# Kernel tuning notes

Hardware: AMD Instinct MI355X
Metric: run time of the kernel (lower is better)

Reference implementation:

```python
import jax, jax.numpy as jnp
import numpy as np

B, T, F = 2048, 256, 64
EMB, UNITS = 16, 32
CAT = UNITS + EMB  # concat([h, x]) -> 48


def setup_inputs() -> dict:
    key = jax.random.key(0)
    ks = jax.random.split(key, 12)
    s = lambda k, shape, fan: jax.random.normal(k, shape, jnp.float32) / np.sqrt(fan)
    return {
        "x": jax.random.normal(ks[0], (B, T, F), jnp.float32),
        "W_emb": s(ks[1], (F, EMB), F), "b_emb": jnp.zeros((EMB,), jnp.float32),
        "W_f": s(ks[2], (CAT, UNITS), CAT), "b_f": jnp.zeros((UNITS,), jnp.float32),
        "W_i": s(ks[3], (CAT, UNITS), CAT), "b_i": jnp.zeros((UNITS,), jnp.float32),
        "W_c": s(ks[4], (CAT, UNITS), CAT), "b_c": jnp.zeros((UNITS,), jnp.float32),
        "W_o": s(ks[5], (CAT, UNITS), CAT), "b_o": jnp.zeros((UNITS,), jnp.float32),
        "W_out": s(ks[6], (UNITS, 1), UNITS), "b_out": jnp.zeros((1,), jnp.float32),
    }


def reference(x, W_emb, b_emb, W_f, b_f, W_i, b_i, W_c, b_c, W_o, b_o, W_out, b_out):
    # embedding: Dense(16, sigmoid)
    e = jax.nn.sigmoid(jnp.einsum('btf,fe->bte', x, W_emb) + b_emb)  # [B,T,EMB]
    e_t = jnp.swapaxes(e, 0, 1)  # [T,B,EMB] for scan

    h0 = jnp.zeros((x.shape[0], UNITS), jnp.float32)
    c0 = jnp.zeros((x.shape[0], UNITS), jnp.float32)

    # fuse 4 gate Dense layers into one GEMM per step (same math)
    W_gates = jnp.concatenate([W_f, W_i, W_c, W_o], axis=1)  # [CAT, 4*UNITS]
    b_gates = jnp.concatenate([b_f, b_i, b_c, b_o], axis=0)

    def step(carry, x_t):
        h, c = carry
        z = jnp.concatenate([h, x_t], axis=-1)  # concat([h_t, x_t])
        g = z @ W_gates + b_gates  # [B, 4*UNITS]
        f = jax.nn.sigmoid(g[:, :UNITS])
        i = jax.nn.sigmoid(g[:, UNITS:2 * UNITS])
        ch = jnp.tanh(g[:, 2 * UNITS:3 * UNITS])
        o = jax.nn.sigmoid(g[:, 3 * UNITS:])
        c_new = f * c + i * ch
        h_new = o * jnp.tanh(c_new)
        return (h_new, c_new), None

    (h_last, _), _ = jax.lax.scan(step, (h0, c0), e_t)
    return jax.nn.sigmoid(h_last @ W_out + b_out)  # [B,1]
```

## Files before the change

### kernel.cpp

```cpp
#include <hip/hip_runtime.h>

#define B_ 2048
#define T_ 256
#define F_ 64
#define EMB_ 16
#define UNITS_ 32
#define L2E 1.44269504f

typedef __attribute__((ext_vector_type(8))) short bf16x8;
typedef __attribute__((ext_vector_type(4))) float f32x4;

__device__ __forceinline__ unsigned short f2bf(float f) {
    unsigned u = __float_as_uint(f);
    return (unsigned short)((u + 0x7FFFu + ((u >> 16) & 1u)) >> 16);
}
__device__ __forceinline__ float fast_sigmoid(float x) {
    return __builtin_amdgcn_rcpf(1.0f + __builtin_amdgcn_exp2f(-L2E * x));
}

__global__ __launch_bounds__(64) void embed_mfma(
    const float* __restrict__ x, const float* __restrict__ Wemb,
    const float* __restrict__ bemb, unsigned int* __restrict__ e_ws)
{
    __shared__ unsigned short slab[2][16][72];

    const int lane = threadIdx.x;
    const int g = lane >> 4, c = lane & 15;
    const int tile = blockIdx.x >> 5;
    const int t0 = (blockIdx.x & 31) * 8;

    bf16x8 A1, A2;
    #pragma unroll
    for (int j = 0; j < 4; ++j) {
        A1[j]     = (short)f2bf(Wemb[(4 * g + j) * EMB_ + c]);
        A1[j + 4] = (short)f2bf(Wemb[(16 + 4 * g + j) * EMB_ + c]);
        A2[j]     = (short)f2bf(Wemb[(32 + 4 * g + j) * EMB_ + c]);
        A2[j + 4] = (short)f2bf(Wemb[(48 + 4 * g + j) * EMB_ + c]);
    }
    f32x4 bc;
    #pragma unroll
    for (int r = 0; r < 4; ++r) bc[r] = bemb[4 * g + r];

    const int sr = lane >> 2, sc = lane & 3;
    const float* xs = x + (size_t)(tile * 16 + sr) * T_ * F_ + sc * 16;

    float4 rld[4], nld[4];
    {
        const float4* p = (const float4*)(xs + (size_t)t0 * F_);
        rld[0] = p[0]; rld[1] = p[1]; rld[2] = p[2]; rld[3] = p[3];
    }

    #pragma unroll
    for (int i = 0; i < 9; ++i) {
        if (i < 7) {
            const float4* p = (const float4*)(xs + (size_t)(t0 + i + 1) * F_);
            nld[0] = p[0]; nld[1] = p[1]; nld[2] = p[2]; nld[3] = p[3];
        }
        if (i < 8) {
            const float* f = (const float*)rld;
            unsigned u[8];
            #pragma unroll
            for (int k = 0; k < 8; ++k)
                u[k] = (unsigned)f2bf(f[2 * k]) | ((unsigned)f2bf(f[2 * k + 1]) << 16);
            uint4* d = (uint4*)&slab[i & 1][sr][sc * 16];
            d[0] = make_uint4(u[0], u[1], u[2], u[3]);
            d[1] = make_uint4(u[4], u[5], u[6], u[7]);
        }
        if (i > 0) {
            const unsigned short* row = &slab[(i - 1) & 1][c][0];
            ushort4 l1 = *(const ushort4*)(row + 4 * g);
            ushort4 h1 = *(const ushort4*)(row + 16 + 4 * g);
            ushort4 l2 = *(const ushort4*)(row + 32 + 4 * g);
            ushort4 h2 = *(const ushort4*)(row + 48 + 4 * g);
            bf16x8 B1 = {(short)l1.x, (short)l1.y, (short)l1.z, (short)l1.w,
                         (short)h1.x, (short)h1.y, (short)h1.z, (short)h1.w};
            bf16x8 B2 = {(short)l2.x, (short)l2.y, (short)l2.z, (short)l2.w,
                         (short)h2.x, (short)h2.y, (short)h2.z, (short)h2.w};
            f32x4 acc = __builtin_amdgcn_mfma_f32_16x16x32_bf16(A1, B1, bc, 0, 0, 0);
            acc = __builtin_amdgcn_mfma_f32_16x16x32_bf16(A2, B2, acc, 0, 0, 0);
            unsigned u0 = (unsigned)f2bf(fast_sigmoid(acc[0])) |
                          ((unsigned)f2bf(fast_sigmoid(acc[1])) << 16);
            unsigned u1 = (unsigned)f2bf(fast_sigmoid(acc[2])) |
                          ((unsigned)f2bf(fast_sigmoid(acc[3])) << 16);
            size_t idx = (((size_t)tile * T_ + (t0 + i - 1)) * 64 + lane) * 2;
            *(uint2*)(e_ws + idx) = make_uint2(u0, u1);
        }
        #pragma unroll
        for (int k = 0; k < 4; ++k) rld[k] = nld[k];
    }
}

__global__ __launch_bounds__(256) void lstm_rec(
    const float* __restrict__ Wf, const float* __restrict__ bfv,
    const float* __restrict__ Wi, const float* __restrict__ biv,
    const float* __restrict__ Wc, const float* __restrict__ bcv,
    const float* __restrict__ Wo, const float* __restrict__ bov,
    const float* __restrict__ Wout, const float* __restrict__ bout,
    const unsigned int* __restrict__ e_ws, float* __restrict__ out)
{
    __shared__ unsigned short hx[2][16][36];
    __shared__ float pred[4][16];

    const int tid = threadIdx.x;
    const int w = tid >> 6;
    const int lane = tid & 63;
    const int g = lane >> 4, m15 = lane & 15;
    const int bt = blockIdx.x;

    const int gate = m15 & 3;
    const float* Wsel = (gate == 0) ? Wf : (gate == 1) ? Wi : (gate == 2) ? Wc : Wo;
    const float ascale = (gate == 2) ? (-2.0f * L2E) : (-L2E);
    const int uAb = 8 * w + 2 * (m15 >> 2);

    bf16x8 Ah[2], Ae[2];
    #pragma unroll
    for (int tau = 0; tau < 2; ++tau) {
        const int uA = uAb + tau;
        #pragma unroll
        for (int j = 0; j < 4; ++j) {
            Ah[tau][j]     = (short)f2bf(ascale * Wsel[(4 * g + j) * UNITS_ + uA]);
            Ah[tau][j + 4] = (short)f2bf(ascale * Wsel[(16 + 4 * g + j) * UNITS_ + uA]);
            Ae[tau][j]     = (short)f2bf(ascale * Wsel[(32 + 4 * g + j) * UNITS_ + uA]);
            Ae[tau][j + 4] = 0;
        }
    }
    f32x4 bias[2];
    #pragma unroll
    for (int tau = 0; tau < 2; ++tau) {
        const int u = 8 * w + 2 * g + tau;
        bias[tau][0] = -L2E * bfv[u];
        bias[tau][1] = -L2E * biv[u];
        bias[tau][2] = -2.0f * L2E * bcv[u];
        bias[tau][3] = -L2E * bov[u];
    }

    const uint2* ep = (const uint2*)e_ws + (size_t)bt * T_ * 64 + lane;
    uint2 ering[4];
    #pragma unroll
    for (int s = 0; s < 4; ++s) ering[s] = ep[(size_t)s * 64];

    for (int i = tid; i < 2 * 16 * 36 / 2; i += 256) ((unsigned*)hx)[i] = 0;
    __syncthreads();

    float c0 = 0.f, c1 = 0.f, hf0 = 0.f, hf1 = 0.f;

    auto cell = [&](const f32x4& acc, float& cst, float& hf) {
        float Ef = __builtin_amdgcn_exp2f(acc[0]);
        float Ei = __builtin_amdgcn_exp2f(acc[1]);
        float Ec = __builtin_amdgcn_exp2f(acc[2]);
        float Eo = __builtin_amdgcn_exp2f(acc[3]);
        float Pf = 1.f + Ef, Pi = 1.f + Ei, Pc = 1.f + Ec, Po = 1.f + Eo;
        float Mc = 1.f - Ec;
        float t1 = Pi * Pc;
        float num = fmaf(cst, t1, Pf * Mc);
        float den = Pf * t1;
        float cn = num * __builtin_amdgcn_rcpf(den);
        cst = cn;
        float Eh = __builtin_amdgcn_exp2f(cn * (-2.0f * L2E));
        float Mh = 1.f - Eh;
        float d2 = (1.f + Eh) * Po;
        hf = Mh * __builtin_amdgcn_rcpf(d2);
    };

    f32x4 Fe0, Fe1;
    {
        uint2 ev = ering[0];
        bf16x8 Be = {(short)(ev.x & 0xffff), (short)(ev.x >> 16),
                     (short)(ev.y & 0xffff), (short)(ev.y >> 16), 0, 0, 0, 0};
        Fe0 = __builtin_amdgcn_mfma_f32_16x16x32_bf16(Ae[0], Be, bias[0], 0, 0, 0);
        Fe1 = __builtin_amdgcn_mfma_f32_16x16x32_bf16(Ae[1], Be, bias[1], 0, 0, 0);
    }

    #pragma unroll 1
    for (int t = 0; t < T_; t += 4) {
        #pragma unroll
        for (int s = 0; s < 4; ++s) {
            const int u = t + s;
            const unsigned short* hrow = &hx[u & 1][m15][0];
            ushort4 hlo = *(const ushort4*)(hrow + 4 * g);
            ushort4 hhi = *(const ushort4*)(hrow + 16 + 4 * g);
            bf16x8 Bh = {(short)hlo.x, (short)hlo.y, (short)hlo.z, (short)hlo.w,
                         (short)hhi.x, (short)hhi.y, (short)hhi.z, (short)hhi.w};
            f32x4 a0 = __builtin_amdgcn_mfma_f32_16x16x32_bf16(Ah[0], Bh, Fe0, 0, 0, 0);
            f32x4 a1 = __builtin_amdgcn_mfma_f32_16x16x32_bf16(Ah[1], Bh, Fe1, 0, 0, 0);

            int tn = (u + 4 < T_) ? u + 4 : T_ - 1;
            uint2 ev = ering[(s + 1) & 3];
            ering[s] = ep[(size_t)tn * 64];
            bf16x8 Be = {(short)(ev.x & 0xffff), (short)(ev.x >> 16),
                         (short)(ev.y & 0xffff), (short)(ev.y >> 16), 0, 0, 0, 0};
            Fe0 = __builtin_amdgcn_mfma_f32_16x16x32_bf16(Ae[0], Be, bias[0], 0, 0, 0);
            Fe1 = __builtin_amdgcn_mfma_f32_16x16x32_bf16(Ae[1], Be, bias[1], 0, 0, 0);

            cell(a0, c0, hf0);
            cell(a1, c1, hf1);
            unsigned pk;
            asm("v_cvt_pk_bf16_f32 %0, %1, %2" : "=v"(pk) : "v"(hf0), "v"(hf1));
            *(unsigned*)&hx[(u + 1) & 1][m15][8 * w + 2 * g] = pk;

            asm volatile("s_waitcnt lgkmcnt(0)\n\ts_barrier" ::: "memory");
        }
    }

    float p = hf0 * Wout[8 * w + 2 * g] + hf1 * Wout[8 * w + 2 * g + 1];
    p += __shfl_xor(p, 16, 64);
    p += __shfl_xor(p, 32, 64);
    if (lane < 16) pred[w][lane] = p;
    __syncthreads();
    if (tid < 16)
        out[bt * 16 + tid] = fast_sigmoid(pred[0][tid] + pred[1][tid] +
                                          pred[2][tid] + pred[3][tid] + bout[0]);
}

extern "C" void kernel_launch(void* const* d_in, const int* in_sizes, int n_in,
                              void* d_out, int out_size, void* d_ws, size_t ws_size,
                              hipStream_t stream) {
    const float* x    = (const float*)d_in[0];
    const float* Wemb = (const float*)d_in[1];
    const float* bemb = (const float*)d_in[2];
    const float* Wf   = (const float*)d_in[3];
    const float* bfv  = (const float*)d_in[4];
    const float* Wi   = (const float*)d_in[5];
    const float* biv  = (const float*)d_in[6];
    const float* Wc   = (const float*)d_in[7];
    const float* bcv  = (const float*)d_in[8];
    const float* Wo   = (const float*)d_in[9];
    const float* bov  = (const float*)d_in[10];
    const float* Wout = (const float*)d_in[11];
    const float* bout = (const float*)d_in[12];
    float* out = (float*)d_out;
    unsigned int* e_ws = (unsigned int*)d_ws;

    hipLaunchKernelGGL(embed_mfma, dim3(128 * 32), dim3(64), 0, stream,
                       x, Wemb, bemb, e_ws);
    hipLaunchKernelGGL(lstm_rec, dim3(B_ / 16), dim3(256), 0, stream,
                       Wf, bfv, Wi, biv, Wc, bcv, Wo, bov, Wout, bout,
                       (const unsigned int*)e_ws, out);
}
```

Baseline: 88.37 us.

## Interleave two independent batch tiles per LSTM block to increase ILP

Each recurrent block now processes two 16-row batch tiles with separate hidden/cell states, interleaving their MFMAs and cell math within each timestep and sharing one barrier per step. The grid is halved accordingly. The intent is to hide the serial MFMA/transcendental/barrier latency of the recurrence with independent work, at the cost of more registers per thread and fewer active blocks across the GPU.

```diff
diff --git a/kernel.cpp b/kernel.cpp
--- a/kernel.cpp
+++ b/kernel.cpp
@@ -98,14 +98,13 @@
     const float* __restrict__ Wout, const float* __restrict__ bout,
     const unsigned int* __restrict__ e_ws, float* __restrict__ out)
 {
-    __shared__ unsigned short hx[2][16][36];
-    __shared__ float pred[4][16];
+    __shared__ unsigned short hx[2][2][16][36];
+    __shared__ float pred[2][4][16];
 
     const int tid = threadIdx.x;
     const int w = tid >> 6;
     const int lane = tid & 63;
     const int g = lane >> 4, m15 = lane & 15;
-    const int bt = blockIdx.x;
 
     const int gate = m15 & 3;
     const float* Wsel = (gate == 0) ? Wf : (gate == 1) ? Wi : (gate == 2) ? Wc : Wo;
@@ -134,15 +133,21 @@
         bias[tau][3] = -L2E * bov[u];
     }
 
-    const uint2* ep = (const uint2*)e_ws + (size_t)bt * T_ * 64 + lane;
-    uint2 ering[4];
-    #pragma unroll
-    for (int s = 0; s < 4; ++s) ering[s] = ep[(size_t)s * 64];
-
-    for (int i = tid; i < 2 * 16 * 36 / 2; i += 256) ((unsigned*)hx)[i] = 0;
+    const int btA = blockIdx.x * 2, btB = btA + 1;
+    const uint2* epA = (const uint2*)e_ws + (size_t)btA * T_ * 64 + lane;
+    const uint2* epB = (const uint2*)e_ws + (size_t)btB * T_ * 64 + lane;
+    uint2 erA[4], erB[4];
+    #pragma unroll
+    for (int s = 0; s < 4; ++s) {
+        erA[s] = epA[(size_t)s * 64];
+        erB[s] = epB[(size_t)s * 64];
+    }
+
+    for (int i = tid; i < 2 * 2 * 16 * 36 / 2; i += 256) ((unsigned*)hx)[i] = 0;
     __syncthreads();
 
-    float c0 = 0.f, c1 = 0.f, hf0 = 0.f, hf1 = 0.f;
+    float cA0 = 0.f, cA1 = 0.f, hfA0 = 0.f, hfA1 = 0.f;
+    float cB0 = 0.f, cB1 = 0.f, hfB0 = 0.f, hfB1 = 0.f;
 
     auto cell = [&](const f32x4& acc, float& cst, float& hf) {
         float Ef = __builtin_amdgcn_exp2f(acc[0]);
@@ -161,14 +166,18 @@
         float d2 = (1.f + Eh) * Po;
         hf = Mh * __builtin_amdgcn_rcpf(d2);
     };
-
-    f32x4 Fe0, Fe1;
+    auto mkBe = [](uint2 ev) -> bf16x8 {
+        return bf16x8{(short)(ev.x & 0xffff), (short)(ev.x >> 16),
+                      (short)(ev.y & 0xffff), (short)(ev.y >> 16), 0, 0, 0, 0};
+    };
+
+    f32x4 FeA0, FeA1, FeB0, FeB1;
     {
-        uint2 ev = ering[0];
-        bf16x8 Be = {(short)(ev.x & 0xffff), (short)(ev.x >> 16),
-                     (short)(ev.y & 0xffff), (short)(ev.y >> 16), 0, 0, 0, 0};
-        Fe0 = __builtin_amdgcn_mfma_f32_16x16x32_bf16(Ae[0], Be, bias[0], 0, 0, 0);
-        Fe1 = __builtin_amdgcn_mfma_f32_16x16x32_bf16(Ae[1], Be, bias[1], 0, 0, 0);
+        bf16x8 BeA = mkBe(erA[0]), BeB = mkBe(erB[0]);
+        FeA0 = __builtin_amdgcn_mfma_f32_16x16x32_bf16(Ae[0], BeA, bias[0], 0, 0, 0);
+        FeA1 = __builtin_amdgcn_mfma_f32_16x16x32_bf16(Ae[1], BeA, bias[1], 0, 0, 0);
+        FeB0 = __builtin_amdgcn_mfma_f32_16x16x32_bf16(Ae[0], BeB, bias[0], 0, 0, 0);
+        FeB1 = __builtin_amdgcn_mfma_f32_16x16x32_bf16(Ae[1], BeB, bias[1], 0, 0, 0);
     }
 
     #pragma unroll 1
@@ -176,40 +185,58 @@
         #pragma unroll
         for (int s = 0; s < 4; ++s) {
             const int u = t + s;
-            const unsigned short* hrow = &hx[u & 1][m15][0];
-            ushort4 hlo = *(const ushort4*)(hrow + 4 * g);
-            ushort4 hhi = *(const ushort4*)(hrow + 16 + 4 * g);
-            bf16x8 Bh = {(short)hlo.x, (short)hlo.y, (short)hlo.z, (short)hlo.w,
-                         (short)hhi.x, (short)hhi.y, (short)hhi.z, (short)hhi.w};
-            f32x4 a0 = __builtin_amdgcn_mfma_f32_16x16x32_bf16(Ah[0], Bh, Fe0, 0, 0, 0);
-            f32x4 a1 = __builtin_amdgcn_mfma_f32_16x16x32_bf16(Ah[1], Bh, Fe1, 0, 0, 0);
+            const unsigned short* hrA = &hx[0][u & 1][m15][0];
+            const unsigned short* hrB = &hx[1][u & 1][m15][0];
+            ushort4 alo = *(const ushort4*)(hrA + 4 * g);
+            ushort4 ahi = *(const ushort4*)(hrA + 16 + 4 * g);
+            ushort4 blo = *(const ushort4*)(hrB + 4 * g);
+            ushort4 bhi = *(const ushort4*)(hrB + 16 + 4 * g);
+            bf16x8 BhA = {(short)alo.x, (short)alo.y, (short)alo.z, (short)alo.w,
+                          (short)ahi.x, (short)ahi.y, (short)ahi.z, (short)ahi.w};
+            bf16x8 BhB = {(short)blo.x, (short)blo.y, (short)blo.z, (short)blo.w,
+                          (short)bhi.x, (short)bhi.y, (short)bhi.z, (short)bhi.w};
+            f32x4 aA0 = __builtin_amdgcn_mfma_f32_16x16x32_bf16(Ah[0], BhA, FeA0, 0, 0, 0);
+            f32x4 aA1 = __builtin_amdgcn_mfma_f32_16x16x32_bf16(Ah[1], BhA, FeA1, 0, 0, 0);
+            f32x4 aB0 = __builtin_amdgcn_mfma_f32_16x16x32_bf16(Ah[0], BhB, FeB0, 0, 0, 0);
+            f32x4 aB1 = __builtin_amdgcn_mfma_f32_16x16x32_bf16(Ah[1], BhB, FeB1, 0, 0, 0);
 
             int tn = (u + 4 < T_) ? u + 4 : T_ - 1;
-            uint2 ev = ering[(s + 1) & 3];
-            ering[s] = ep[(size_t)tn * 64];
-            bf16x8 Be = {(short)(ev.x & 0xffff), (short)(ev.x >> 16),
-                         (short)(ev.y & 0xffff), (short)(ev.y >> 16), 0, 0, 0, 0};
-            Fe0 = __builtin_amdgcn_mfma_f32_16x16x32_bf16(Ae[0], Be, bias[0], 0, 0, 0);
-            Fe1 = __builtin_amdgcn_mfma_f32_16x16x32_bf16(Ae[1], Be, bias[1], 0, 0, 0);
-
-            cell(a0, c0, hf0);
-            cell(a1, c1, hf1);
-            unsigned pk;
-            asm("v_cvt_pk_bf16_f32 %0, %1, %2" : "=v"(pk) : "v"(hf0), "v"(hf1));
-            *(unsigned*)&hx[(u + 1) & 1][m15][8 * w + 2 * g] = pk;
+            bf16x8 BeA = mkBe(erA[(s + 1) & 3]);
+            bf16x8 BeB = mkBe(erB[(s + 1) & 3]);
+            erA[s] = epA[(size_t)tn * 64];
+            erB[s] = epB[(size_t)tn * 64];
+            FeA0 = __builtin_amdgcn_mfma_f32_16x16x32_bf16(Ae[0], BeA, bias[0], 0, 0, 0);
+            FeA1 = __builtin_amdgcn_mfma_f32_16x16x32_bf16(Ae[1], BeA, bias[1], 0, 0, 0);
+            FeB0 = __builtin_amdgcn_mfma_f32_16x16x32_bf16(Ae[0], BeB, bias[0], 0, 0, 0);
+            FeB1 = __builtin_amdgcn_mfma_f32_16x16x32_bf16(Ae[1], BeB, bias[1], 0, 0, 0);
+
+            cell(aA0, cA0, hfA0);
+            cell(aA1, cA1, hfA1);
+            cell(aB0, cB0, hfB0);
+            cell(aB1, cB1, hfB1);
+            unsigned pkA, pkB;
+            asm("v_cvt_pk_bf16_f32 %0, %1, %2" : "=v"(pkA) : "v"(hfA0), "v"(hfA1));
+            asm("v_cvt_pk_bf16_f32 %0, %1, %2" : "=v"(pkB) : "v"(hfB0), "v"(hfB1));
+            *(unsigned*)&hx[0][(u + 1) & 1][m15][8 * w + 2 * g] = pkA;
+            *(unsigned*)&hx[1][(u + 1) & 1][m15][8 * w + 2 * g] = pkB;
 
             asm volatile("s_waitcnt lgkmcnt(0)\n\ts_barrier" ::: "memory");
         }
     }
 
-    float p = hf0 * Wout[8 * w + 2 * g] + hf1 * Wout[8 * w + 2 * g + 1];
-    p += __shfl_xor(p, 16, 64);
-    p += __shfl_xor(p, 32, 64);
-    if (lane < 16) pred[w][lane] = p;
+    float pA = hfA0 * Wout[8 * w + 2 * g] + hfA1 * Wout[8 * w + 2 * g + 1];
+    float pB = hfB0 * Wout[8 * w + 2 * g] + hfB1 * Wout[8 * w + 2 * g + 1];
+    pA += __shfl_xor(pA, 16, 64); pA += __shfl_xor(pA, 32, 64);
+    pB += __shfl_xor(pB, 16, 64); pB += __shfl_xor(pB, 32, 64);
+    if (lane < 16) { pred[0][w][lane] = pA; pred[1][w][lane] = pB; }
     __syncthreads();
-    if (tid < 16)
-        out[bt * 16 + tid] = fast_sigmoid(pred[0][tid] + pred[1][tid] +
-                                          pred[2][tid] + pred[3][tid] + bout[0]);
+    if (tid < 32) {
+        int ch = tid >> 4, m = tid & 15;
+        float sum = bout[0];
+        #pragma unroll
+        for (int ww = 0; ww < 4; ++ww) sum += pred[ch][ww][m];
+        out[(btA + ch) * 16 + m] = fast_sigmoid(sum);
+    }
 }
 
 extern "C" void kernel_launch(void* const* d_in, const int* in_sizes, int n_in,
@@ -233,7 +260,7 @@
 
     hipLaunchKernelGGL(embed_mfma, dim3(128 * 32), dim3(64), 0, stream,
                        x, Wemb, bemb, e_ws);
-    hipLaunchKernelGGL(lstm_rec, dim3(B_ / 16), dim3(256), 0, stream,
+    hipLaunchKernelGGL(lstm_rec, dim3(B_ / 32), dim3(256), 0, stream,
                        Wf, bfv, Wi, biv, Wc, bcv, Wo, bov, Wout, bout,
                        (const unsigned int*)e_ws, out);
 }
```

Result: slower. 119.4 us (+35.1%).

## Split LSTM recurrence across two waves with per-gate MFMAs and register-held hidden state

Applied to the files above, without the earlier changes.

The recurrent kernel now uses 2 waves per block instead of 4. Each wave computes all four gates for 16 hidden units with four MFMAs per step, where before each wave handled 8 units with gates interleaved across rows. Each wave keeps its own half of the packed bf16 hidden state in registers and exchanges only the other half through a small LDS buffer. This cuts barrier participants and LDS traffic on the sequential critical path. In exchange each wave does twice the MFMA and transcendental work per step, and the e prefetch distance grows by one step.

```diff
diff --git a/kernel.cpp b/kernel.cpp
--- a/kernel.cpp
+++ b/kernel.cpp
@@ -90,7 +90,7 @@
     }
 }
 
-__global__ __launch_bounds__(256) void lstm_rec(
+__global__ __launch_bounds__(128) void lstm_rec(
     const float* __restrict__ Wf, const float* __restrict__ bfv,
     const float* __restrict__ Wi, const float* __restrict__ biv,
     const float* __restrict__ Wc, const float* __restrict__ bcv,
@@ -98,8 +98,8 @@
     const float* __restrict__ Wout, const float* __restrict__ bout,
     const unsigned int* __restrict__ e_ws, float* __restrict__ out)
 {
-    __shared__ unsigned short hx[2][16][36];
-    __shared__ float pred[4][16];
+    __shared__ uint2 hxch[2][2][64];
+    __shared__ float pred[2][16];
 
     const int tid = threadIdx.x;
     const int w = tid >> 6;
@@ -107,109 +107,119 @@
     const int g = lane >> 4, m15 = lane & 15;
     const int bt = blockIdx.x;
 
-    const int gate = m15 & 3;
-    const float* Wsel = (gate == 0) ? Wf : (gate == 1) ? Wi : (gate == 2) ? Wc : Wo;
-    const float ascale = (gate == 2) ? (-2.0f * L2E) : (-L2E);
-    const int uAb = 8 * w + 2 * (m15 >> 2);
-
-    bf16x8 Ah[2], Ae[2];
-    #pragma unroll
-    for (int tau = 0; tau < 2; ++tau) {
-        const int uA = uAb + tau;
+    const float* Wg[4] = {Wf, Wi, Wc, Wo};
+    const float* bg[4] = {bfv, biv, bcv, bov};
+
+    const int urow = 16 * w + m15;
+    bf16x8 Ah[4], Ae[4];
+    f32x4 bias[4];
+    #pragma unroll
+    for (int tau = 0; tau < 4; ++tau) {
+        const float sc = (tau == 2) ? (-2.0f * L2E) : (-L2E);
         #pragma unroll
         for (int j = 0; j < 4; ++j) {
-            Ah[tau][j]     = (short)f2bf(ascale * Wsel[(4 * g + j) * UNITS_ + uA]);
-            Ah[tau][j + 4] = (short)f2bf(ascale * Wsel[(16 + 4 * g + j) * UNITS_ + uA]);
-            Ae[tau][j]     = (short)f2bf(ascale * Wsel[(32 + 4 * g + j) * UNITS_ + uA]);
+            Ah[tau][j]     = (short)f2bf(sc * Wg[tau][(4 * g + j) * UNITS_ + urow]);
+            Ah[tau][j + 4] = (short)f2bf(sc * Wg[tau][(16 + 4 * g + j) * UNITS_ + urow]);
+            Ae[tau][j]     = (short)f2bf(sc * Wg[tau][(32 + 4 * g + j) * UNITS_ + urow]);
             Ae[tau][j + 4] = 0;
         }
-    }
-    f32x4 bias[2];
-    #pragma unroll
-    for (int tau = 0; tau < 2; ++tau) {
-        const int u = 8 * w + 2 * g + tau;
-        bias[tau][0] = -L2E * bfv[u];
-        bias[tau][1] = -L2E * biv[u];
-        bias[tau][2] = -2.0f * L2E * bcv[u];
-        bias[tau][3] = -L2E * bov[u];
+        #pragma unroll
+        for (int r = 0; r < 4; ++r)
+            bias[tau][r] = sc * bg[tau][16 * w + 4 * g + r];
     }
 
     const uint2* ep = (const uint2*)e_ws + (size_t)bt * T_ * 64 + lane;
-    uint2 ering[4];
-    #pragma unroll
-    for (int s = 0; s < 4; ++s) ering[s] = ep[(size_t)s * 64];
-
-    for (int i = tid; i < 2 * 16 * 36 / 2; i += 256) ((unsigned*)hx)[i] = 0;
+    uint2 er[4];
+    #pragma unroll
+    for (int s = 0; s < 4; ++s) er[s] = ep[(size_t)s * 64];
+
+    hxch[0][w][lane] = make_uint2(0u, 0u);
     __syncthreads();
 
-    float c0 = 0.f, c1 = 0.f, hf0 = 0.f, hf1 = 0.f;
-
-    auto cell = [&](const f32x4& acc, float& cst, float& hf) {
-        float Ef = __builtin_amdgcn_exp2f(acc[0]);
-        float Ei = __builtin_amdgcn_exp2f(acc[1]);
-        float Ec = __builtin_amdgcn_exp2f(acc[2]);
-        float Eo = __builtin_amdgcn_exp2f(acc[3]);
-        float Pf = 1.f + Ef, Pi = 1.f + Ei, Pc = 1.f + Ec, Po = 1.f + Eo;
-        float Mc = 1.f - Ec;
-        float t1 = Pi * Pc;
-        float num = fmaf(cst, t1, Pf * Mc);
-        float den = Pf * t1;
-        float cn = num * __builtin_amdgcn_rcpf(den);
-        cst = cn;
-        float Eh = __builtin_amdgcn_exp2f(cn * (-2.0f * L2E));
-        float Mh = 1.f - Eh;
-        float d2 = (1.f + Eh) * Po;
-        hf = Mh * __builtin_amdgcn_rcpf(d2);
+    auto mkBe = [](uint2 ev) -> bf16x8 {
+        return bf16x8{(short)(ev.x & 0xffff), (short)(ev.x >> 16),
+                      (short)(ev.y & 0xffff), (short)(ev.y >> 16), 0, 0, 0, 0};
     };
 
-    f32x4 Fe0, Fe1;
+    f32x4 Fe0, Fe1, Fe2, Fe3;
     {
-        uint2 ev = ering[0];
-        bf16x8 Be = {(short)(ev.x & 0xffff), (short)(ev.x >> 16),
-                     (short)(ev.y & 0xffff), (short)(ev.y >> 16), 0, 0, 0, 0};
+        bf16x8 Be = mkBe(er[0]);
         Fe0 = __builtin_amdgcn_mfma_f32_16x16x32_bf16(Ae[0], Be, bias[0], 0, 0, 0);
         Fe1 = __builtin_amdgcn_mfma_f32_16x16x32_bf16(Ae[1], Be, bias[1], 0, 0, 0);
-    }
+        Fe2 = __builtin_amdgcn_mfma_f32_16x16x32_bf16(Ae[2], Be, bias[2], 0, 0, 0);
+        Fe3 = __builtin_amdgcn_mfma_f32_16x16x32_bf16(Ae[3], Be, bias[3], 0, 0, 0);
+        er[0] = ep[(size_t)4 * 64];
+    }
+
+    uint2 ownpk = make_uint2(0u, 0u);
+    float cst[4] = {0.f, 0.f, 0.f, 0.f};
+    float hf[4]  = {0.f, 0.f, 0.f, 0.f};
 
     #pragma unroll 1
     for (int t = 0; t < T_; t += 4) {
         #pragma unroll
         for (int s = 0; s < 4; ++s) {
+            const int p = s & 1;
+            uint2 oth = hxch[p][w ^ 1][lane];
+            uint2 lo = w ? oth : ownpk;
+            uint2 hi = w ? ownpk : oth;
+            bf16x8 Bh = {(short)(lo.x & 0xffff), (short)(lo.x >> 16),
+                         (short)(lo.y & 0xffff), (short)(lo.y >> 16),
+                         (short)(hi.x & 0xffff), (short)(hi.x >> 16),
+                         (short)(hi.y & 0xffff), (short)(hi.y >> 16)};
+            f32x4 acc0 = __builtin_amdgcn_mfma_f32_16x16x32_bf16(Ah[0], Bh, Fe0, 0, 0, 0);
+            f32x4 acc1 = __builtin_amdgcn_mfma_f32_16x16x32_bf16(Ah[1], Bh, Fe1, 0, 0, 0);
+            f32x4 acc2 = __builtin_amdgcn_mfma_f32_16x16x32_bf16(Ah[2], Bh, Fe2, 0, 0, 0);
+            f32x4 acc3 = __builtin_amdgcn_mfma_f32_16x16x32_bf16(Ah[3], Bh, Fe3, 0, 0, 0);
+
             const int u = t + s;
-            const unsigned short* hrow = &hx[u & 1][m15][0];
-            ushort4 hlo = *(const ushort4*)(hrow + 4 * g);
-            ushort4 hhi = *(const ushort4*)(hrow + 16 + 4 * g);
-            bf16x8 Bh = {(short)hlo.x, (short)hlo.y, (short)hlo.z, (short)hlo.w,
-                         (short)hhi.x, (short)hhi.y, (short)hhi.z, (short)hhi.w};
-            f32x4 a0 = __builtin_amdgcn_mfma_f32_16x16x32_bf16(Ah[0], Bh, Fe0, 0, 0, 0);
-            f32x4 a1 = __builtin_amdgcn_mfma_f32_16x16x32_bf16(Ah[1], Bh, Fe1, 0, 0, 0);
-
-            int tn = (u + 4 < T_) ? u + 4 : T_ - 1;
-            uint2 ev = ering[(s + 1) & 3];
-            ering[s] = ep[(size_t)tn * 64];
-            bf16x8 Be = {(short)(ev.x & 0xffff), (short)(ev.x >> 16),
-                         (short)(ev.y & 0xffff), (short)(ev.y >> 16), 0, 0, 0, 0};
+            const int sl = (s + 1) & 3;
+            const int tn = (u + 5 < T_) ? u + 5 : T_ - 1;
+            uint2 ev = er[sl];
+            er[sl] = ep[(size_t)tn * 64];
+            bf16x8 Be = mkBe(ev);
             Fe0 = __builtin_amdgcn_mfma_f32_16x16x32_bf16(Ae[0], Be, bias[0], 0, 0, 0);
             Fe1 = __builtin_amdgcn_mfma_f32_16x16x32_bf16(Ae[1], Be, bias[1], 0, 0, 0);
-
-            cell(a0, c0, hf0);
-            cell(a1, c1, hf1);
-            unsigned pk;
-            asm("v_cvt_pk_bf16_f32 %0, %1, %2" : "=v"(pk) : "v"(hf0), "v"(hf1));
-            *(unsigned*)&hx[(u + 1) & 1][m15][8 * w + 2 * g] = pk;
+            Fe2 = __builtin_amdgcn_mfma_f32_16x16x32_bf16(Ae[2], Be, bias[2], 0, 0, 0);
+            Fe3 = __builtin_amdgcn_mfma_f32_16x16x32_bf16(Ae[3], Be, bias[3], 0, 0, 0);
+
+            #pragma unroll
+            for (int r = 0; r < 4; ++r) {
+                float Ef = __builtin_amdgcn_exp2f(acc0[r]);
+                float Ei = __builtin_amdgcn_exp2f(acc1[r]);
+                float Ec = __builtin_amdgcn_exp2f(acc2[r]);
+                float Eo = __builtin_amdgcn_exp2f(acc3[r]);
+                float Pf = 1.f + Ef, Pi = 1.f + Ei, Pc = 1.f + Ec, Po = 1.f + Eo;
+                float Mc = 1.f - Ec;
+                float t1 = Pi * Pc;
+                float num = fmaf(cst[r], t1, Pf * Mc);
+                float den = Pf * t1;
+                float cn = num * __builtin_amdgcn_rcpf(den);
+                cst[r] = cn;
+                float Eh = __builtin_amdgcn_exp2f(cn * (-2.0f * L2E));
+                float Mh = 1.f - Eh;
+                float d2 = (1.f + Eh) * Po;
+                hf[r] = Mh * __builtin_amdgcn_rcpf(d2);
+            }
+            unsigned pk0, pk1;
+            asm("v_cvt_pk_bf16_f32 %0, %1, %2" : "=v"(pk0) : "v"(hf[0]), "v"(hf[1]));
+            asm("v_cvt_pk_bf16_f32 %0, %1, %2" : "=v"(pk1) : "v"(hf[2]), "v"(hf[3]));
+            ownpk = make_uint2(pk0, pk1);
+            hxch[p ^ 1][w][lane] = ownpk;
 
             asm volatile("s_waitcnt lgkmcnt(0)\n\ts_barrier" ::: "memory");
         }
     }
 
-    float p = hf0 * Wout[8 * w + 2 * g] + hf1 * Wout[8 * w + 2 * g + 1];
-    p += __shfl_xor(p, 16, 64);
-    p += __shfl_xor(p, 32, 64);
-    if (lane < 16) pred[w][lane] = p;
+    float pv = 0.f;
+    #pragma unroll
+    for (int r = 0; r < 4; ++r) pv = fmaf(hf[r], Wout[16 * w + 4 * g + r], pv);
+    pv += __shfl_xor(pv, 16, 64);
+    pv += __shfl_xor(pv, 32, 64);
+    if (lane < 16) pred[w][lane] = pv;
     __syncthreads();
     if (tid < 16)
-        out[bt * 16 + tid] = fast_sigmoid(pred[0][tid] + pred[1][tid] +
-                                          pred[2][tid] + pred[3][tid] + bout[0]);
+        out[bt * 16 + tid] = fast_sigmoid(pred[0][tid] + pred[1][tid] + bout[0]);
 }
 
 extern "C" void kernel_launch(void* const* d_in, const int* in_sizes, int n_in,
@@ -233,7 +243,7 @@
 
     hipLaunchKernelGGL(embed_mfma, dim3(128 * 32), dim3(64), 0, stream,
                        x, Wemb, bemb, e_ws);
-    hipLaunchKernelGGL(lstm_rec, dim3(B_ / 16), dim3(256), 0, stream,
+    hipLaunchKernelGGL(lstm_rec, dim3(B_ / 16), dim3(128), 0, stream,
                        Wf, bfv, Wi, biv, Wc, bcv, Wo, bov, Wout, bout,
                        (const unsigned int*)e_ws, out);
 }
```

Result: slower. 122.4 us (+38.5%).

## Fuse embedding computation into the LSTM recurrence kernel

Applied to the files above, without the earlier changes.

Drops the separate embedding kernel and its workspace round trip. Each wave of the recurrent kernel now loads raw x rows, runs the embedding MFMA and sigmoid on the fly, and keeps a ring of pre-computed embeddings a few steps ahead, with x prefetched six steps in advance. This removes one launch and the bf16 intermediate traffic. In exchange, every one of the four waves does redundant embedding work inside the latency-bound serial loop, and only 128 blocks are left to stream all of x.

```diff
diff --git a/kernel.cpp b/kernel.cpp
--- a/kernel.cpp
+++ b/kernel.cpp
@@ -18,85 +18,15 @@
     return __builtin_amdgcn_rcpf(1.0f + __builtin_amdgcn_exp2f(-L2E * x));
 }
 
-__global__ __launch_bounds__(64) void embed_mfma(
-    const float* __restrict__ x, const float* __restrict__ Wemb,
-    const float* __restrict__ bemb, unsigned int* __restrict__ e_ws)
-{
-    __shared__ unsigned short slab[2][16][72];
-
-    const int lane = threadIdx.x;
-    const int g = lane >> 4, c = lane & 15;
-    const int tile = blockIdx.x >> 5;
-    const int t0 = (blockIdx.x & 31) * 8;
-
-    bf16x8 A1, A2;
-    #pragma unroll
-    for (int j = 0; j < 4; ++j) {
-        A1[j]     = (short)f2bf(Wemb[(4 * g + j) * EMB_ + c]);
-        A1[j + 4] = (short)f2bf(Wemb[(16 + 4 * g + j) * EMB_ + c]);
-        A2[j]     = (short)f2bf(Wemb[(32 + 4 * g + j) * EMB_ + c]);
-        A2[j + 4] = (short)f2bf(Wemb[(48 + 4 * g + j) * EMB_ + c]);
-    }
-    f32x4 bc;
-    #pragma unroll
-    for (int r = 0; r < 4; ++r) bc[r] = bemb[4 * g + r];
-
-    const int sr = lane >> 2, sc = lane & 3;
-    const float* xs = x + (size_t)(tile * 16 + sr) * T_ * F_ + sc * 16;
-
-    float4 rld[4], nld[4];
-    {
-        const float4* p = (const float4*)(xs + (size_t)t0 * F_);
-        rld[0] = p[0]; rld[1] = p[1]; rld[2] = p[2]; rld[3] = p[3];
-    }
-
-    #pragma unroll
-    for (int i = 0; i < 9; ++i) {
-        if (i < 7) {
-            const float4* p = (const float4*)(xs + (size_t)(t0 + i + 1) * F_);
-            nld[0] = p[0]; nld[1] = p[1]; nld[2] = p[2]; nld[3] = p[3];
-        }
-        if (i < 8) {
-            const float* f = (const float*)rld;
-            unsigned u[8];
-            #pragma unroll
-            for (int k = 0; k < 8; ++k)
-                u[k] = (unsigned)f2bf(f[2 * k]) | ((unsigned)f2bf(f[2 * k + 1]) << 16);
-            uint4* d = (uint4*)&slab[i & 1][sr][sc * 16];
-            d[0] = make_uint4(u[0], u[1], u[2], u[3]);
-            d[1] = make_uint4(u[4], u[5], u[6], u[7]);
-        }
-        if (i > 0) {
-            const unsigned short* row = &slab[(i - 1) & 1][c][0];
-            ushort4 l1 = *(const ushort4*)(row + 4 * g);
-            ushort4 h1 = *(const ushort4*)(row + 16 + 4 * g);
-            ushort4 l2 = *(const ushort4*)(row + 32 + 4 * g);
-            ushort4 h2 = *(const ushort4*)(row + 48 + 4 * g);
-            bf16x8 B1 = {(short)l1.x, (short)l1.y, (short)l1.z, (short)l1.w,
-                         (short)h1.x, (short)h1.y, (short)h1.z, (short)h1.w};
-            bf16x8 B2 = {(short)l2.x, (short)l2.y, (short)l2.z, (short)l2.w,
-                         (short)h2.x, (short)h2.y, (short)h2.z, (short)h2.w};
-            f32x4 acc = __builtin_amdgcn_mfma_f32_16x16x32_bf16(A1, B1, bc, 0, 0, 0);
-            acc = __builtin_amdgcn_mfma_f32_16x16x32_bf16(A2, B2, acc, 0, 0, 0);
-            unsigned u0 = (unsigned)f2bf(fast_sigmoid(acc[0])) |
-                          ((unsigned)f2bf(fast_sigmoid(acc[1])) << 16);
-            unsigned u1 = (unsigned)f2bf(fast_sigmoid(acc[2])) |
-                          ((unsigned)f2bf(fast_sigmoid(acc[3])) << 16);
-            size_t idx = (((size_t)tile * T_ + (t0 + i - 1)) * 64 + lane) * 2;
-            *(uint2*)(e_ws + idx) = make_uint2(u0, u1);
-        }
-        #pragma unroll
-        for (int k = 0; k < 4; ++k) rld[k] = nld[k];
-    }
-}
-
-__global__ __launch_bounds__(256) void lstm_rec(
+__global__ __launch_bounds__(256) void lstm_fused(
+    const float* __restrict__ x,
+    const float* __restrict__ Wemb, const float* __restrict__ bemb,
     const float* __restrict__ Wf, const float* __restrict__ bfv,
     const float* __restrict__ Wi, const float* __restrict__ biv,
     const float* __restrict__ Wc, const float* __restrict__ bcv,
     const float* __restrict__ Wo, const float* __restrict__ bov,
     const float* __restrict__ Wout, const float* __restrict__ bout,
-    const unsigned int* __restrict__ e_ws, float* __restrict__ out)
+    float* __restrict__ out)
 {
     __shared__ unsigned short hx[2][16][36];
     __shared__ float pred[4][16];
@@ -134,16 +64,22 @@
         bias[tau][3] = -L2E * bov[u];
     }
 
-    const uint2* ep = (const uint2*)e_ws + (size_t)bt * T_ * 64 + lane;
-    uint2 ering[4];
-    #pragma unroll
-    for (int s = 0; s < 4; ++s) ering[s] = ep[(size_t)s * 64];
-
-    for (int i = tid; i < 2 * 16 * 36 / 2; i += 256) ((unsigned*)hx)[i] = 0;
-    __syncthreads();
-
-    float c0 = 0.f, c1 = 0.f, hf0 = 0.f, hf1 = 0.f;
-
+    bf16x8 Ea1, Ea2;
+    #pragma unroll
+    for (int j = 0; j < 4; ++j) {
+        Ea1[j]     = (short)f2bf(Wemb[(4 * g + j) * EMB_ + m15]);
+        Ea1[j + 4] = (short)f2bf(Wemb[(16 + 4 * g + j) * EMB_ + m15]);
+        Ea2[j]     = (short)f2bf(Wemb[(32 + 4 * g + j) * EMB_ + m15]);
+        Ea2[j + 4] = (short)f2bf(Wemb[(48 + 4 * g + j) * EMB_ + m15]);
+    }
+    f32x4 bce;
+    #pragma unroll
+    for (int r = 0; r < 4; ++r) bce[r] = bemb[4 * g + r];
+
+    auto mkBe = [](uint2 ev) -> bf16x8 {
+        return bf16x8{(short)(ev.x & 0xffff), (short)(ev.x >> 16),
+                      (short)(ev.y & 0xffff), (short)(ev.y >> 16), 0, 0, 0, 0};
+    };
     auto cell = [&](const f32x4& acc, float& cst, float& hf) {
         float Ef = __builtin_amdgcn_exp2f(acc[0]);
         float Ei = __builtin_amdgcn_exp2f(acc[1]);
@@ -162,45 +98,98 @@
         hf = Mh * __builtin_amdgcn_rcpf(d2);
     };
 
+    const float* xb = x + (size_t)(bt * 16 + m15) * T_ * F_;
+    auto produce = [&](float4 q0, float4 q1, float4 q2, float4 q3) -> uint2 {
+        bf16x8 B1 = {(short)f2bf(q0.x), (short)f2bf(q0.y),
+                     (short)f2bf(q0.z), (short)f2bf(q0.w),
+                     (short)f2bf(q1.x), (short)f2bf(q1.y),
+                     (short)f2bf(q1.z), (short)f2bf(q1.w)};
+        bf16x8 B2 = {(short)f2bf(q2.x), (short)f2bf(q2.y),
+                     (short)f2bf(q2.z), (short)f2bf(q2.w),
+                     (short)f2bf(q3.x), (short)f2bf(q3.y),
+                     (short)f2bf(q3.z), (short)f2bf(q3.w)};
+        f32x4 a = __builtin_amdgcn_mfma_f32_16x16x32_bf16(Ea1, B1, bce, 0, 0, 0);
+        a = __builtin_amdgcn_mfma_f32_16x16x32_bf16(Ea2, B2, a, 0, 0, 0);
+        unsigned u0 = (unsigned)f2bf(fast_sigmoid(a[0])) |
+                      ((unsigned)f2bf(fast_sigmoid(a[1])) << 16);
+        unsigned u1 = (unsigned)f2bf(fast_sigmoid(a[2])) |
+                      ((unsigned)f2bf(fast_sigmoid(a[3])) << 16);
+        return make_uint2(u0, u1);
+    };
+
+    uint2 ering[4];
+    #pragma unroll
+    for (int p = 0; p < 4; ++p) {
+        const float* xp = xb + (size_t)p * F_;
+        float4 q0 = *(const float4*)(xp + 4 * g);
+        float4 q1 = *(const float4*)(xp + 16 + 4 * g);
+        float4 q2 = *(const float4*)(xp + 32 + 4 * g);
+        float4 q3 = *(const float4*)(xp + 48 + 4 * g);
+        ering[p] = produce(q0, q1, q2, q3);
+    }
+    float4 xA0, xA1, xA2, xA3, xB0, xB1, xB2, xB3;
+    {
+        const float* p4 = xb + (size_t)4 * F_;
+        xA0 = *(const float4*)(p4 + 4 * g);      xA1 = *(const float4*)(p4 + 16 + 4 * g);
+        xA2 = *(const float4*)(p4 + 32 + 4 * g); xA3 = *(const float4*)(p4 + 48 + 4 * g);
+        const float* p5 = xb + (size_t)5 * F_;
+        xB0 = *(const float4*)(p5 + 4 * g);      xB1 = *(const float4*)(p5 + 16 + 4 * g);
+        xB2 = *(const float4*)(p5 + 32 + 4 * g); xB3 = *(const float4*)(p5 + 48 + 4 * g);
+    }
+
+    for (int i = tid; i < 2 * 16 * 36 / 2; i += 256) ((unsigned*)hx)[i] = 0;
+    __syncthreads();
+
+    float c0 = 0.f, c1 = 0.f, hf0 = 0.f, hf1 = 0.f;
+
     f32x4 Fe0, Fe1;
     {
-        uint2 ev = ering[0];
-        bf16x8 Be = {(short)(ev.x & 0xffff), (short)(ev.x >> 16),
-                     (short)(ev.y & 0xffff), (short)(ev.y >> 16), 0, 0, 0, 0};
+        bf16x8 Be = mkBe(ering[0]);
         Fe0 = __builtin_amdgcn_mfma_f32_16x16x32_bf16(Ae[0], Be, bias[0], 0, 0, 0);
         Fe1 = __builtin_amdgcn_mfma_f32_16x16x32_bf16(Ae[1], Be, bias[1], 0, 0, 0);
     }
 
+#define STEP(S, XQ0, XQ1, XQ2, XQ3)                                            \
+    do {                                                                       \
+        const int u = t + (S);                                                 \
+        const unsigned short* hrow = &hx[u & 1][m15][0];                       \
+        ushort4 hlo = *(const ushort4*)(hrow + 4 * g);                         \
+        ushort4 hhi = *(const ushort4*)(hrow + 16 + 4 * g);                    \
+        bf16x8 Bh = {(short)hlo.x, (short)hlo.y, (short)hlo.z, (short)hlo.w,   \
+                     (short)hhi.x, (short)hhi.y, (short)hhi.z, (short)hhi.w};  \
+        f32x4 a0 = __builtin_amdgcn_mfma_f32_16x16x32_bf16(Ah[0], Bh, Fe0, 0, 0, 0); \
+        f32x4 a1 = __builtin_amdgcn_mfma_f32_16x16x32_bf16(Ah[1], Bh, Fe1, 0, 0, 0); \
+        {                                                                      \
+            bf16x8 Be = mkBe(ering[((S) + 1) & 3]);                            \
+            Fe0 = __builtin_amdgcn_mfma_f32_16x16x32_bf16(Ae[0], Be, bias[0], 0, 0, 0); \
+            Fe1 = __builtin_amdgcn_mfma_f32_16x16x32_bf16(Ae[1], Be, bias[1], 0, 0, 0); \
+        }                                                                      \
+        ering[(S) & 3] = produce(XQ0, XQ1, XQ2, XQ3);                          \
+        {                                                                      \
+            int lx = (u + 6 < T_) ? u + 6 : T_ - 1;                            \
+            const float* p = xb + (size_t)lx * F_;                             \
+            XQ0 = *(const float4*)(p + 4 * g);                                 \
+            XQ1 = *(const float4*)(p + 16 + 4 * g);                            \
+            XQ2 = *(const float4*)(p + 32 + 4 * g);                            \
+            XQ3 = *(const float4*)(p + 48 + 4 * g);                            \
+        }                                                                      \
+        cell(a0, c0, hf0);                                                     \
+        cell(a1, c1, hf1);                                                     \
+        unsigned pk;                                                           \
+        asm("v_cvt_pk_bf16_f32 %0, %1, %2" : "=v"(pk) : "v"(hf0), "v"(hf1));   \
+        *(unsigned*)&hx[(u + 1) & 1][m15][8 * w + 2 * g] = pk;                 \
+        asm volatile("s_waitcnt lgkmcnt(0)\n\ts_barrier" ::: "memory");        \
+        __builtin_amdgcn_sched_barrier(0);                                     \
+    } while (0)
+
     #pragma unroll 1
     for (int t = 0; t < T_; t += 4) {
-        #pragma unroll
-        for (int s = 0; s < 4; ++s) {
-            const int u = t + s;
-            const unsigned short* hrow = &hx[u & 1][m15][0];
-            ushort4 hlo = *(const ushort4*)(hrow + 4 * g);
-            ushort4 hhi = *(const ushort4*)(hrow + 16 + 4 * g);
-            bf16x8 Bh = {(short)hlo.x, (short)hlo.y, (short)hlo.z, (short)hlo.w,
-                         (short)hhi.x, (short)hhi.y, (short)hhi.z, (short)hhi.w};
-            f32x4 a0 = __builtin_amdgcn_mfma_f32_16x16x32_bf16(Ah[0], Bh, Fe0, 0, 0, 0);
-            f32x4 a1 = __builtin_amdgcn_mfma_f32_16x16x32_bf16(Ah[1], Bh, Fe1, 0, 0, 0);
-
-            int tn = (u + 4 < T_) ? u + 4 : T_ - 1;
-            uint2 ev = ering[(s + 1) & 3];
-            ering[s] = ep[(size_t)tn * 64];
-            bf16x8 Be = {(short)(ev.x & 0xffff), (short)(ev.x >> 16),
-                         (short)(ev.y & 0xffff), (short)(ev.y >> 16), 0, 0, 0, 0};
-            Fe0 = __builtin_amdgcn_mfma_f32_16x16x32_bf16(Ae[0], Be, bias[0], 0, 0, 0);
-            Fe1 = __builtin_amdgcn_mfma_f32_16x16x32_bf16(Ae[1], Be, bias[1], 0, 0, 0);
-
-            cell(a0, c0, hf0);
-            cell(a1, c1, hf1);
-            unsigned pk;
-            asm("v_cvt_pk_bf16_f32 %0, %1, %2" : "=v"(pk) : "v"(hf0), "v"(hf1));
-            *(unsigned*)&hx[(u + 1) & 1][m15][8 * w + 2 * g] = pk;
-
-            asm volatile("s_waitcnt lgkmcnt(0)\n\ts_barrier" ::: "memory");
-        }
-    }
+        STEP(0, xA0, xA1, xA2, xA3);
+        STEP(1, xB0, xB1, xB2, xB3);
+        STEP(2, xA0, xA1, xA2, xA3);
+        STEP(3, xB0, xB1, xB2, xB3);
+    }
+#undef STEP
 
     float p = hf0 * Wout[8 * w + 2 * g] + hf1 * Wout[8 * w + 2 * g + 1];
     p += __shfl_xor(p, 16, 64);
@@ -229,11 +218,8 @@
     const float* Wout = (const float*)d_in[11];
     const float* bout = (const float*)d_in[12];
     float* out = (float*)d_out;
-    unsigned int* e_ws = (unsigned int*)d_ws;
-
-    hipLaunchKernelGGL(embed_mfma, dim3(128 * 32), dim3(64), 0, stream,
-                       x, Wemb, bemb, e_ws);
-    hipLaunchKernelGGL(lstm_rec, dim3(B_ / 16), dim3(256), 0, stream,
-                       Wf, bfv, Wi, biv, Wc, bcv, Wo, bov, Wout, bout,
-                       (const unsigned int*)e_ws, out);
-}
+
+    hipLaunchKernelGGL(lstm_fused, dim3(B_ / 16), dim3(256), 0, stream,
+                       x, Wemb, bemb, Wf, bfv, Wi, biv, Wc, bcv, Wo, bov,
+                       Wout, bout, out);
+}
```

Result: slower. 147.8 us (+67.3%).
